# Performance work log

Hardware: AMD Instinct MI355X
Metric: run time of the kernel (lower is better)

The kernel has to match this reference:

```python
import jax, jax.numpy as jnp
import numpy as np

NUM_FEATURES = 256   # 2**8
BOND_DIM = 16
N_CORES = 8          # log2(NUM_FEATURES)
BATCH = 262144


def _mpo_cores(mpo_weights, n, bond_dim):
    # Slice the flat parameter vector into n cores of shape (l, r, 2, 2).
    shapes = [(1, bond_dim, 2, 2)] + [(bond_dim, bond_dim, 2, 2)] * (n - 2) + [(bond_dim, 1, 2, 2)]
    cores, off = [], 0
    for s in shapes:
        sz = int(np.prod(s))
        cores.append(mpo_weights[off:off + sz].reshape(s))
        off += sz
    return cores


def _contract_mpo(cores):
    # Sequentially contract the tensor-train cores into the full (2^n, 2^n) matrix.
    # T has axes (bond, I, J) where I/J accumulate the row/col physical bits
    # in order i1..in / j1..jn, matching the original einsum + reshape.
    T = cores[0][0]          # (r, 2, 2)
    dim = 2
    for A in cores[1:]:      # A: (l, r2, 2, 2)
        T = jnp.einsum('aIJ,abkm->bIkJm', T, A).reshape(A.shape[1], dim * 2, dim * 2)
        dim *= 2
    return T[0]              # (2^n, 2^n)


def setup_inputs() -> dict:
    key = jax.random.key(0)
    k1, k2, k3 = jax.random.split(key, 3)
    total = 2 * 4 * BOND_DIM + (N_CORES - 2) * 4 * BOND_DIM ** 2  # 6272
    return {
        'x': jax.random.normal(k1, (BATCH, NUM_FEATURES), dtype=jnp.float32),
        'mpo_weights': jax.random.normal(k2, (total,), dtype=jnp.float32) * 0.1,
        'dense_kernel': jax.random.normal(k3, (NUM_FEATURES, 1), dtype=jnp.float32) * 0.1,
        'dense_bias': jnp.zeros((1,), dtype=jnp.float32),
    }


def reference(x, mpo_weights, dense_kernel, dense_bias):
    W = _contract_mpo(_mpo_cores(mpo_weights, N_CORES, BOND_DIM))  # (256, 256)
    h = jnp.square(x @ W)                                          # (B, 256)
    return h @ dense_kernel + dense_bias                           # (B, 1)
```

## Files before the change

kernel.cpp:

```cpp
#include <hip/hip_runtime.h>
#include <hip/hip_bf16.h>

typedef _Float16 half8 __attribute__((ext_vector_type(8)));
typedef float    floatx4 __attribute__((ext_vector_type(4)));

#define WSCALE      4096.0f
#define WSCALE_INV  (1.0f/(4096.0f*4096.0f))

#define S0_OFF   0
#define S1_OFF   256
#define S2_OFF   4352
#define S3_OFF   8448
#define T1_OFF   8704
#define T2_OFF   12800
#define WF16_OFF 78336

__global__ void mpo_pairs(const float* __restrict__ w, float* __restrict__ ws) {
    int idx = blockIdx.x * blockDim.x + threadIdx.x;
    int p, base, r, outoff;
    if      (idx < 256)  { p = 0; base = 0;    r = 16; outoff = S0_OFF; }
    else if (idx < 4352) { p = 1; base = 256;  r = 16; outoff = S1_OFF; }
    else if (idx < 8448) { p = 2; base = 4352; r = 16; outoff = S2_OFF; }
    else if (idx < 8704) { p = 3; base = 8448; r = 1;  outoff = S3_OFF; }
    else return;
    int li = idx - base;
    int mm = li & 3, kk = (li >> 2) & 3, ac = li >> 4;
    int c = ac % r, a = ac / r;
    int k1 = kk >> 1, k2 = kk & 1, m1 = mm >> 1, m2 = mm & 1;
    const int coreoff[8] = {0, 64, 1088, 2112, 3136, 4160, 5184, 6208};
    const float* A = w + coreoff[2 * p];
    const float* B = w + coreoff[2 * p + 1];
    float s = 0.f;
    for (int b = 0; b < 16; ++b)
        s += A[((a * 16 + b) * 2 + k1) * 2 + m1] * B[((b * r + c) * 2 + k2) * 2 + m2];
    ws[outoff + li] = s;
}

__global__ void mpo_step(const float* __restrict__ T, const float* __restrict__ S,
                         float* __restrict__ out, int r, int dim) {
    int idx = blockIdx.x * blockDim.x + threadIdx.x;
    int D4 = dim * 4;
    int total = r * D4 * D4;
    if (idx >= total) return;
    int J4 = idx % D4; int t = idx / D4; int I4 = t % D4; int b = t / D4;
    int I = I4 >> 2, k = I4 & 3, J = J4 >> 2, m = J4 & 3;
    float s = 0.f;
    for (int a = 0; a < 16; ++a)
        s += T[(a * dim + I) * dim + J] * S[((a * r + b) * 4 + k) * 4 + m];
    out[idx] = s;
}

__global__ void mpo_step_final(const float* __restrict__ T, const float* __restrict__ S,
                               _Float16* __restrict__ Wf) {
    int idx = blockIdx.x * blockDim.x + threadIdx.x;
    int J4 = idx & 255; int I4 = idx >> 8;
    int I = I4 >> 2, k = I4 & 3, J = J4 >> 2, m = J4 & 3;
    float s = 0.f;
    for (int a = 0; a < 16; ++a)
        s += T[(a * 64 + I) * 64 + J] * S[(a * 4 + k) * 4 + m];
    int n = J4 >> 4, lr = J4 & 15, kk = I4 >> 5, gg = (I4 >> 3) & 3, j = I4 & 7;
    Wf[(((n * 8 + kk) * 64) + gg * 16 + lr) * 8 + j] = (_Float16)(s * WSCALE);
}

__global__ __launch_bounds__(1024, 4)
void mpo_main(const float* __restrict__ x, const _Float16* __restrict__ Wf,
              const float* __restrict__ dk, const float* __restrict__ bias,
              float* __restrict__ out) {
    extern __shared__ _Float16 Wl[];

    const int tid  = threadIdx.x;
    const int lane = tid & 63;
    const int wave = tid >> 6;
    const int lrow = lane & 15;
    const int g    = lane >> 4;

    {
        const floatx4* src = reinterpret_cast<const floatx4*>(Wf);
        floatx4* dst = reinterpret_cast<floatx4*>(Wl);
#pragma unroll
        for (int i = 0; i < 8; ++i)
            dst[tid + i * 1024] = src[tid + i * 1024];
    }
    const float bs = bias[0];
    __syncthreads();

    const long blockbase = (long)blockIdx.x * 1024;
    const half8* Wv = reinterpret_cast<const half8*>(Wl);
    const float* dkl = dk + lrow;

#define SB()    __builtin_amdgcn_sched_barrier(0)

#pragma unroll 1
    for (int pass = 0; pass < 4; ++pass) {
        const long wrow = blockbase + pass * 256 + wave * 16;

        half8 a[8];
        floatx4 lo[4], hi[4];
        const float* xb = x + (wrow + lrow) * 256 + g * 8;

#define XLD(i)  do { const float* p_ = xb + (i) * 32;                                    \
                     lo[(i) & 3] = *reinterpret_cast<const floatx4*>(p_);                \
                     hi[(i) & 3] = *reinterpret_cast<const floatx4*>(p_ + 4); } while (0)
#define XCVT(i) do { half8 f_;                                                           \
                     f_[0] = (_Float16)lo[(i) & 3][0]; f_[1] = (_Float16)lo[(i) & 3][1]; \
                     f_[2] = (_Float16)lo[(i) & 3][2]; f_[3] = (_Float16)lo[(i) & 3][3]; \
                     f_[4] = (_Float16)hi[(i) & 3][0]; f_[5] = (_Float16)hi[(i) & 3][1]; \
                     f_[6] = (_Float16)hi[(i) & 3][2]; f_[7] = (_Float16)hi[(i) & 3][3]; \
                     a[(i)] = f_; } while (0)

        XLD(0); XLD(1); XLD(2); XLD(3); SB();
        XCVT(0); XLD(4); SB();
        XCVT(1); XLD(5); SB();
        XCVT(2); XLD(6); SB();
        XCVT(3); XLD(7); SB();
        XCVT(4); XCVT(5); XCVT(6); XCVT(7); SB();

        float rp[4] = {0, 0, 0, 0};

#pragma unroll 1
        for (int n = 0; n < 16; ++n) {
            const float kv = dkl[n * 16];
            const half8* Wn = Wv + n * 512 + lane;
            floatx4 c0 = {0, 0, 0, 0}, c1 = {0, 0, 0, 0};
#pragma unroll
            for (int kk = 0; kk < 8; kk += 2) {
                half8 b0 = Wn[kk * 64];
                half8 b1 = Wn[kk * 64 + 64];
                c0 = __builtin_amdgcn_mfma_f32_16x16x32_f16(a[kk],     b0, c0, 0, 0, 0);
                c1 = __builtin_amdgcn_mfma_f32_16x16x32_f16(a[kk + 1], b1, c1, 0, 0, 0);
            }
#pragma unroll
            for (int r = 0; r < 4; ++r) {
                float y = c0[r] + c1[r];
                rp[r] += y * y * kv;
            }
        }

#pragma unroll
        for (int r = 0; r < 4; ++r) {
            float v = rp[r];
            v += __shfl_xor(v, 1);
            v += __shfl_xor(v, 2);
            v += __shfl_xor(v, 4);
            v += __shfl_xor(v, 8);
            rp[r] = v;
        }
        if (lrow == 0) {
            floatx4 o;
#pragma unroll
            for (int r = 0; r < 4; ++r) o[r] = rp[r] * WSCALE_INV + bs;
            *reinterpret_cast<floatx4*>(out + wrow + g * 4) = o;
        }
    }
}

extern "C" void kernel_launch(void* const* d_in, const int* in_sizes, int n_in,
                              void* d_out, int out_size, void* d_ws, size_t ws_size,
                              hipStream_t stream) {
    const float* x    = (const float*)d_in[0];
    const float* w    = (const float*)d_in[1];
    const float* dk   = (const float*)d_in[2];
    const float* bias = (const float*)d_in[3];
    float* out = (float*)d_out;
    float* ws  = (float*)d_ws;

    _Float16* Wf16 = (_Float16*)(ws + WF16_OFF);

    static bool attr_set = false;
    if (!attr_set) {
        hipFuncSetAttribute((const void*)mpo_main,
                            hipFuncAttributeMaxDynamicSharedMemorySize, 131072);
        attr_set = true;
    }

    mpo_pairs<<<(8704 + 255) / 256, 256, 0, stream>>>(w, ws);
    mpo_step<<<(4096 + 255) / 256, 256, 0, stream>>>(ws + S0_OFF, ws + S1_OFF, ws + T1_OFF, 16, 4);
    mpo_step<<<(65536 + 255) / 256, 256, 0, stream>>>(ws + T1_OFF, ws + S2_OFF, ws + T2_OFF, 16, 16);
    mpo_step_final<<<(65536 + 255) / 256, 256, 0, stream>>>(ws + T2_OFF, ws + S3_OFF, Wf16);

    mpo_main<<<256, 1024, 131072, stream>>>(x, Wf16, dk, bias, out);
}
```

Before: 71.85 us.

## Fuse MPO prep into one kernel and software-pipeline x loads in main

The four small weight-contraction kernels are merged into a single one-block kernel with block-wide barriers between stages, which cuts launch overhead but runs all the prep work on one workgroup. The main kernel now uses 512 threads per block over 8 passes and prefetches the next tile of x into registers while the current tile's MFMAs run. It also stages the dense kernel in LDS and drops the dual accumulator chain in favour of one serial MFMA chain. The extra register pressure and the serialized MFMA dependency could offset the gain from overlapping loads.

```diff
diff --git a/kernel.cpp b/kernel.cpp
--- a/kernel.cpp
+++ b/kernel.cpp
@@ -15,58 +15,71 @@
 #define T2_OFF   12800
 #define WF16_OFF 78336
 
-__global__ void mpo_pairs(const float* __restrict__ w, float* __restrict__ ws) {
-    int idx = blockIdx.x * blockDim.x + threadIdx.x;
-    int p, base, r, outoff;
-    if      (idx < 256)  { p = 0; base = 0;    r = 16; outoff = S0_OFF; }
-    else if (idx < 4352) { p = 1; base = 256;  r = 16; outoff = S1_OFF; }
-    else if (idx < 8448) { p = 2; base = 4352; r = 16; outoff = S2_OFF; }
-    else if (idx < 8704) { p = 3; base = 8448; r = 1;  outoff = S3_OFF; }
-    else return;
-    int li = idx - base;
-    int mm = li & 3, kk = (li >> 2) & 3, ac = li >> 4;
-    int c = ac % r, a = ac / r;
-    int k1 = kk >> 1, k2 = kk & 1, m1 = mm >> 1, m2 = mm & 1;
-    const int coreoff[8] = {0, 64, 1088, 2112, 3136, 4160, 5184, 6208};
-    const float* A = w + coreoff[2 * p];
-    const float* B = w + coreoff[2 * p + 1];
-    float s = 0.f;
-    for (int b = 0; b < 16; ++b)
-        s += A[((a * 16 + b) * 2 + k1) * 2 + m1] * B[((b * r + c) * 2 + k2) * 2 + m2];
-    ws[outoff + li] = s;
+__global__ __launch_bounds__(1024)
+void mpo_prep(const float* __restrict__ w, float* __restrict__ ws,
+              _Float16* __restrict__ Wf) {
+    const int tid = threadIdx.x;
+
+    for (int idx = tid; idx < 8704; idx += 1024) {
+        int p, base, r, outoff;
+        if      (idx < 256)  { p = 0; base = 0;    r = 16; outoff = S0_OFF; }
+        else if (idx < 4352) { p = 1; base = 256;  r = 16; outoff = S1_OFF; }
+        else if (idx < 8448) { p = 2; base = 4352; r = 16; outoff = S2_OFF; }
+        else                 { p = 3; base = 8448; r = 1;  outoff = S3_OFF; }
+        int li = idx - base;
+        int mm = li & 3, kk = (li >> 2) & 3, ac = li >> 4;
+        int c = ac % r, a = ac / r;
+        int k1 = kk >> 1, k2 = kk & 1, m1 = mm >> 1, m2 = mm & 1;
+        const int coreoff[8] = {0, 64, 1088, 2112, 3136, 4160, 5184, 6208};
+        const float* A = w + coreoff[2 * p];
+        const float* B = w + coreoff[2 * p + 1];
+        float s = 0.f;
+        for (int b = 0; b < 16; ++b)
+            s += A[((a * 16 + b) * 2 + k1) * 2 + m1] * B[((b * r + c) * 2 + k2) * 2 + m2];
+        ws[outoff + li] = s;
+    }
+    __threadfence(); __syncthreads();
+
+    for (int idx = tid; idx < 4096; idx += 1024) {
+        const float* T = ws + S0_OFF; const float* S = ws + S1_OFF;
+        int J4 = idx % 16; int t = idx / 16; int I4 = t % 16; int b = t / 16;
+        int I = I4 >> 2, k = I4 & 3, J = J4 >> 2, m = J4 & 3;
+        float s = 0.f;
+        for (int a = 0; a < 16; ++a)
+            s += T[(a * 4 + I) * 4 + J] * S[((a * 16 + b) * 4 + k) * 4 + m];
+        ws[T1_OFF + idx] = s;
+    }
+    __threadfence(); __syncthreads();
+
+    for (int idx = tid; idx < 65536; idx += 1024) {
+        const float* T = ws + T1_OFF; const float* S = ws + S2_OFF;
+        int J4 = idx % 64; int t = idx / 64; int I4 = t % 64; int b = t / 64;
+        int I = I4 >> 2, k = I4 & 3, J = J4 >> 2, m = J4 & 3;
+        float s = 0.f;
+        for (int a = 0; a < 16; ++a)
+            s += T[(a * 16 + I) * 16 + J] * S[((a * 16 + b) * 4 + k) * 4 + m];
+        ws[T2_OFF + idx] = s;
+    }
+    __threadfence(); __syncthreads();
+
+    for (int idx = tid; idx < 65536; idx += 1024) {
+        const float* T = ws + T2_OFF; const float* S = ws + S3_OFF;
+        int J4 = idx & 255; int I4 = idx >> 8;
+        int I = I4 >> 2, k = I4 & 3, J = J4 >> 2, m = J4 & 3;
+        float s = 0.f;
+        for (int a = 0; a < 16; ++a)
+            s += T[(a * 64 + I) * 64 + J] * S[(a * 4 + k) * 4 + m];
+        int n = J4 >> 4, lr = J4 & 15, kk = I4 >> 5, gg = (I4 >> 3) & 3, j = I4 & 7;
+        Wf[(((n * 8 + kk) * 64) + gg * 16 + lr) * 8 + j] = (_Float16)(s * WSCALE);
+    }
 }
 
-__global__ void mpo_step(const float* __restrict__ T, const float* __restrict__ S,
-                         float* __restrict__ out, int r, int dim) {
-    int idx = blockIdx.x * blockDim.x + threadIdx.x;
-    int D4 = dim * 4;
-    int total = r * D4 * D4;
-    if (idx >= total) return;
-    int J4 = idx % D4; int t = idx / D4; int I4 = t % D4; int b = t / D4;
-    int I = I4 >> 2, k = I4 & 3, J = J4 >> 2, m = J4 & 3;
-    float s = 0.f;
-    for (int a = 0; a < 16; ++a)
-        s += T[(a * dim + I) * dim + J] * S[((a * r + b) * 4 + k) * 4 + m];
-    out[idx] = s;
-}
-
-__global__ void mpo_step_final(const float* __restrict__ T, const float* __restrict__ S,
-                               _Float16* __restrict__ Wf) {
-    int idx = blockIdx.x * blockDim.x + threadIdx.x;
-    int J4 = idx & 255; int I4 = idx >> 8;
-    int I = I4 >> 2, k = I4 & 3, J = J4 >> 2, m = J4 & 3;
-    float s = 0.f;
-    for (int a = 0; a < 16; ++a)
-        s += T[(a * 64 + I) * 64 + J] * S[(a * 4 + k) * 4 + m];
-    int n = J4 >> 4, lr = J4 & 15, kk = I4 >> 5, gg = (I4 >> 3) & 3, j = I4 & 7;
-    Wf[(((n * 8 + kk) * 64) + gg * 16 + lr) * 8 + j] = (_Float16)(s * WSCALE);
-}
-
-__global__ __launch_bounds__(1024, 4)
+__global__ __launch_bounds__(512, 2)
 void mpo_main(const float* __restrict__ x, const _Float16* __restrict__ Wf,
               const float* __restrict__ dk, const float* __restrict__ bias,
               float* __restrict__ out) {
     extern __shared__ _Float16 Wl[];
+    float* dkL = reinterpret_cast<float*>(Wl + 65536);
 
     const int tid  = threadIdx.x;
     const int lane = tid & 63;
@@ -74,67 +87,69 @@
     const int lrow = lane & 15;
     const int g    = lane >> 4;
 
+    const long blockbase = (long)blockIdx.x * 1024;
+    const float* xb0 = x + (blockbase + wave * 16 + lrow) * 256 + g * 8;
+
+    half8 a[8];
+    floatx4 lo[8], hi[8];
+
+#define SB()    __builtin_amdgcn_sched_barrier(0)
+#define XLD(i, xn) do { const float* p_ = (xn) + (i) * 32;                     \
+                     lo[i] = *reinterpret_cast<const floatx4*>(p_);            \
+                     hi[i] = *reinterpret_cast<const floatx4*>(p_ + 4); } while (0)
+#define XLD_ALL(xn) do { XLD(0,xn); XLD(1,xn); XLD(2,xn); XLD(3,xn);           \
+                         XLD(4,xn); XLD(5,xn); XLD(6,xn); XLD(7,xn); } while (0)
+#define XCVT(i) do { half8 f_;                                                 \
+                     f_[0] = (_Float16)lo[i][0]; f_[1] = (_Float16)lo[i][1];   \
+                     f_[2] = (_Float16)lo[i][2]; f_[3] = (_Float16)lo[i][3];   \
+                     f_[4] = (_Float16)hi[i][0]; f_[5] = (_Float16)hi[i][1];   \
+                     f_[6] = (_Float16)hi[i][2]; f_[7] = (_Float16)hi[i][3];   \
+                     a[i] = f_; } while (0)
+#define XCVT_ALL() do { XCVT(0); XCVT(1); XCVT(2); XCVT(3);                    \
+                        XCVT(4); XCVT(5); XCVT(6); XCVT(7); } while (0)
+
+    XLD_ALL(xb0);
+    SB();
     {
         const floatx4* src = reinterpret_cast<const floatx4*>(Wf);
         floatx4* dst = reinterpret_cast<floatx4*>(Wl);
 #pragma unroll
-        for (int i = 0; i < 8; ++i)
-            dst[tid + i * 1024] = src[tid + i * 1024];
+        for (int i = 0; i < 16; ++i)
+            dst[tid + i * 512] = src[tid + i * 512];
     }
+    if (tid < 256) dkL[tid] = dk[tid];
     const float bs = bias[0];
     __syncthreads();
 
-    const long blockbase = (long)blockIdx.x * 1024;
+    XCVT_ALL();
+    SB();
+
     const half8* Wv = reinterpret_cast<const half8*>(Wl);
-    const float* dkl = dk + lrow;
-
-#define SB()    __builtin_amdgcn_sched_barrier(0)
 
 #pragma unroll 1
-    for (int pass = 0; pass < 4; ++pass) {
-        const long wrow = blockbase + pass * 256 + wave * 16;
-
-        half8 a[8];
-        floatx4 lo[4], hi[4];
-        const float* xb = x + (wrow + lrow) * 256 + g * 8;
-
-#define XLD(i)  do { const float* p_ = xb + (i) * 32;                                    \
-                     lo[(i) & 3] = *reinterpret_cast<const floatx4*>(p_);                \
-                     hi[(i) & 3] = *reinterpret_cast<const floatx4*>(p_ + 4); } while (0)
-#define XCVT(i) do { half8 f_;                                                           \
-                     f_[0] = (_Float16)lo[(i) & 3][0]; f_[1] = (_Float16)lo[(i) & 3][1]; \
-                     f_[2] = (_Float16)lo[(i) & 3][2]; f_[3] = (_Float16)lo[(i) & 3][3]; \
-                     f_[4] = (_Float16)hi[(i) & 3][0]; f_[5] = (_Float16)hi[(i) & 3][1]; \
-                     f_[6] = (_Float16)hi[(i) & 3][2]; f_[7] = (_Float16)hi[(i) & 3][3]; \
-                     a[(i)] = f_; } while (0)
-
-        XLD(0); XLD(1); XLD(2); XLD(3); SB();
-        XCVT(0); XLD(4); SB();
-        XCVT(1); XLD(5); SB();
-        XCVT(2); XLD(6); SB();
-        XCVT(3); XLD(7); SB();
-        XCVT(4); XCVT(5); XCVT(6); XCVT(7); SB();
+    for (int p = 0; p < 8; ++p) {
+        if (p < 7) {
+            const float* xn = xb0 + (p + 1) * (128 * 256);
+            XLD_ALL(xn);
+        }
+        SB();
 
         float rp[4] = {0, 0, 0, 0};
-
 #pragma unroll 1
         for (int n = 0; n < 16; ++n) {
-            const float kv = dkl[n * 16];
+            const float kv = dkL[n * 16 + lrow];
             const half8* Wn = Wv + n * 512 + lane;
-            floatx4 c0 = {0, 0, 0, 0}, c1 = {0, 0, 0, 0};
+            floatx4 c0 = {0, 0, 0, 0};
 #pragma unroll
-            for (int kk = 0; kk < 8; kk += 2) {
-                half8 b0 = Wn[kk * 64];
-                half8 b1 = Wn[kk * 64 + 64];
-                c0 = __builtin_amdgcn_mfma_f32_16x16x32_f16(a[kk],     b0, c0, 0, 0, 0);
-                c1 = __builtin_amdgcn_mfma_f32_16x16x32_f16(a[kk + 1], b1, c1, 0, 0, 0);
-            }
+            for (int kk = 0; kk < 8; ++kk)
+                c0 = __builtin_amdgcn_mfma_f32_16x16x32_f16(a[kk], Wn[kk * 64], c0, 0, 0, 0);
 #pragma unroll
-            for (int r = 0; r < 4; ++r) {
-                float y = c0[r] + c1[r];
-                rp[r] += y * y * kv;
-            }
+            for (int r = 0; r < 4; ++r)
+                rp[r] += c0[r] * c0[r] * kv;
         }
+
+        if (p < 7) { XCVT_ALL(); }
+        SB();
 
 #pragma unroll
         for (int r = 0; r < 4; ++r) {
@@ -149,7 +164,7 @@
             floatx4 o;
 #pragma unroll
             for (int r = 0; r < 4; ++r) o[r] = rp[r] * WSCALE_INV + bs;
-            *reinterpret_cast<floatx4*>(out + wrow + g * 4) = o;
+            *reinterpret_cast<floatx4*>(out + blockbase + p * 128 + wave * 16 + g * 4) = o;
         }
     }
 }
@@ -169,14 +184,11 @@
     static bool attr_set = false;
     if (!attr_set) {
         hipFuncSetAttribute((const void*)mpo_main,
-                            hipFuncAttributeMaxDynamicSharedMemorySize, 131072);
+                            hipFuncAttributeMaxDynamicSharedMemorySize, 132096);
         attr_set = true;
     }
 
-    mpo_pairs<<<(8704 + 255) / 256, 256, 0, stream>>>(w, ws);
-    mpo_step<<<(4096 + 255) / 256, 256, 0, stream>>>(ws + S0_OFF, ws + S1_OFF, ws + T1_OFF, 16, 4);
-    mpo_step<<<(65536 + 255) / 256, 256, 0, stream>>>(ws + T1_OFF, ws + S2_OFF, ws + T2_OFF, 16, 16);
-    mpo_step_final<<<(65536 + 255) / 256, 256, 0, stream>>>(ws + T2_OFF, ws + S3_OFF, Wf16);
+    mpo_prep<<<1, 1024, 0, stream>>>(w, ws, Wf16);
 
-    mpo_main<<<256, 1024, 131072, stream>>>(x, Wf16, dk, bias, out);
+    mpo_main<<<256, 512, 132096, stream>>>(x, Wf16, dk, bias, out);
 }
```

Result: slower. 222.4 us (+209.6%).
